# Optimization experiments

Measured on AMD Instinct MI355X. Metric: run time of the kernel, lower is better.

## Reference

```python
import jax, jax.numpy as jnp
import numpy as np

B, S, H = 8, 1024, 1024
NH, HD = 16, 64
LN_EPS = 1e-12


def setup_inputs() -> dict:
    key = jax.random.key(0)
    ks = jax.random.split(key, 8)
    sd = 0.02
    return {
        "hidden_states": jax.random.normal(ks[0], (B, S, H), jnp.float32),
        "attention_mask": jnp.zeros((B, 1, 1, S), jnp.float32),
        "Wq": jax.random.normal(ks[1], (H, H), jnp.float32) * sd,
        "bq": jnp.zeros((H,), jnp.float32),
        "Wk": jax.random.normal(ks[2], (H, H), jnp.float32) * sd,
        "bk": jnp.zeros((H,), jnp.float32),
        "Wv": jax.random.normal(ks[3], (H, H), jnp.float32) * sd,
        "bv": jnp.zeros((H,), jnp.float32),
        "Wo": jax.random.normal(ks[4], (H, H), jnp.float32) * sd,
        "bo": jnp.zeros((H,), jnp.float32),
        "ln_gamma": jnp.ones((H,), jnp.float32),
        "ln_beta": jnp.zeros((H,), jnp.float32),
    }


def _heads(x):
    # [B,S,H] -> [B,NH,S,HD]
    return x.reshape(B, S, NH, HD).transpose(0, 2, 1, 3)


def reference(hidden_states, attention_mask, Wq, bq, Wk, bk, Wv, bv, Wo, bo, ln_gamma, ln_beta):
    # QKV projections (torch Linear: x @ W.T + b)
    q = _heads(hidden_states @ Wq.T + bq)
    k = _heads(hidden_states @ Wk.T + bk)
    v = _heads(hidden_states @ Wv.T + bv)
    # scaled dot-product attention with additive mask
    scores = jnp.einsum("bhqd,bhkd->bhqk", q, k) / np.sqrt(HD).astype(np.float32)
    scores = scores + attention_mask  # broadcast [B,1,1,S]
    probs = jax.nn.softmax(scores, axis=-1)
    ctx = jnp.einsum("bhqk,bhkd->bhqd", probs, v)
    ctx = ctx.transpose(0, 2, 1, 3).reshape(B, S, H)
    # output projection + residual + LayerNorm
    out = ctx @ Wo.T + bo
    x = out + hidden_states
    mu = jnp.mean(x, axis=-1, keepdims=True)
    var = jnp.var(x, axis=-1, keepdims=True)
    return (x - mu) * jax.lax.rsqrt(var + LN_EPS) * ln_gamma + ln_beta
```

## Files before the change

kernel.cpp:

```cpp
#include <hip/hip_runtime.h>
#include <stdint.h>

typedef __attribute__((ext_vector_type(8))) __bf16 bf16x8;
typedef __attribute__((ext_vector_type(8))) unsigned short ushortx8;
typedef __attribute__((ext_vector_type(4))) unsigned short ushortx4;
typedef __attribute__((ext_vector_type(4))) short short4v;
typedef __attribute__((ext_vector_type(4))) float floatx4;

#define LOG2E 1.4426950408889634f
#define QSCALE 0.18033688011112043f

#define ASYNC16(g, l) __builtin_amdgcn_global_load_lds( \
    (__attribute__((address_space(1))) void*)(g),       \
    (__attribute__((address_space(3))) void*)(l), 16, 0, 0)

__device__ __forceinline__ unsigned short f2bf(float f) {
    unsigned int u = __float_as_uint(f);
    u += 0x7fffu + ((u >> 16) & 1u);
    return (unsigned short)(u >> 16);
}

__device__ __forceinline__ floatx4 mfma32(bf16x8 a, bf16x8 b, floatx4 c) {
    return __builtin_amdgcn_mfma_f32_16x16x32_bf16(a, b, c, 0, 0, 0);
}
__device__ __forceinline__ floatx4 mfma16(short4v a, short4v b, floatx4 c) {
    return __builtin_amdgcn_mfma_f32_16x16x16bf16_1k(a, b, c, 0, 0, 0);
}

__global__ __launch_bounds__(256) void cvt_all(
    const float* __restrict__ hidden,
    const float* __restrict__ Wq, const float* __restrict__ Wk,
    const float* __restrict__ Wv, const float* __restrict__ Wo,
    unsigned short* __restrict__ hid_bf,
    unsigned short* __restrict__ oqkv, unsigned short* __restrict__ oo)
{
    const float* src;
    unsigned short* dst;
    int i;
    if (blockIdx.x < 4096) {
        src = hidden; dst = hid_bf;
        i = blockIdx.x * 256 + threadIdx.x;
    } else {
        int blk = (blockIdx.x - 4096) >> 9;
        src = (blk == 0) ? Wq : (blk == 1) ? Wk : (blk == 2) ? Wv : Wo;
        dst = (blk == 3) ? oo : oqkv + (size_t)blk * 1048576;
        i = ((blockIdx.x - 4096) & 511) * 256 + threadIdx.x;
    }
    const float4* p = (const float4*)src + (size_t)i * 2;
    float4 a = p[0], b = p[1];
    ushortx8 o;
    o[0] = f2bf(a.x); o[1] = f2bf(a.y); o[2] = f2bf(a.z); o[3] = f2bf(a.w);
    o[4] = f2bf(b.x); o[5] = f2bf(b.y); o[6] = f2bf(b.z); o[7] = f2bf(b.w);
    *((ushortx8*)dst + i) = o;
}

template<bool SWAP>
__device__ __forceinline__ void kloop_bk64(
    const unsigned short* __restrict__ Ag,
    const unsigned short* __restrict__ Wg,
    unsigned short* As, unsigned short* Bs,
    int wm, int wn, int l16, int quad, int t,
    floatx4 acc[4][4])
{
#pragma unroll 1
    for (int k0 = 0; k0 < 1024; k0 += 64) {
        __syncthreads();
#pragma unroll
        for (int i = 0; i < 4; i++) {
            ASYNC16(Ag + (size_t)i * 32 * 1024 + k0, As + i * 2048 + t * 8);
            ASYNC16(Wg + (size_t)i * 32 * 1024 + k0, Bs + i * 2048 + t * 8);
        }
        __syncthreads();
#pragma unroll
        for (int s = 0; s < 2; s++) {
            int pb = ((s * 4 + quad) ^ (l16 & 7)) * 8;
            bf16x8 af[4], bfr[4];
#pragma unroll
            for (int mt = 0; mt < 4; mt++)
                af[mt] = *(const bf16x8*)(As + (wm + mt * 16 + l16) * 64 + pb);
#pragma unroll
            for (int nt = 0; nt < 4; nt++)
                bfr[nt] = *(const bf16x8*)(Bs + (wn + nt * 16 + l16) * 64 + pb);
            if (SWAP) {
#pragma unroll
                for (int ft = 0; ft < 4; ft++)
#pragma unroll
                    for (int st = 0; st < 4; st++)
                        acc[ft][st] = mfma32(bfr[ft], af[st], acc[ft][st]);
            } else {
#pragma unroll
                for (int mt = 0; mt < 4; mt++)
#pragma unroll
                    for (int nt = 0; nt < 4; nt++)
                        acc[mt][nt] = mfma32(af[mt], bfr[nt], acc[mt][nt]);
            }
        }
    }
}

__global__ __launch_bounds__(256) void gemm_qkv(
    const unsigned short* __restrict__ A,
    const unsigned short* __restrict__ W,
    const float* __restrict__ bq, const float* __restrict__ bk, const float* __restrict__ bv,
    unsigned short* __restrict__ Qo, unsigned short* __restrict__ Ko,
    unsigned short* __restrict__ Vo)
{
    __shared__ unsigned short As[128 * 64];
    __shared__ unsigned short Bs[128 * 64];
    const int t = threadIdx.x;
    const int wave = t >> 6, lane = t & 63;
    const int quad = lane >> 4, l16 = lane & 15;
    const int wm = (wave >> 1) * 64, wn = (wave & 1) * 64;
    const int srow = t >> 3;
    const int scol = ((t & 7) ^ (srow & 7)) * 8;

    const unsigned short* Ag = A + ((size_t)blockIdx.x * 128 + srow) * 1024 + scol;
    const unsigned short* Wg = W + ((size_t)blockIdx.y * 128 + srow) * 1024 + scol;

    floatx4 acc[4][4] = {};
    kloop_bk64<true>(Ag, Wg, As, Bs, wm, wn, l16, quad, t, acc);

    int y = blockIdx.y;
    if (y < 16) {
        const float* bp = (y < 8) ? bq : bk;
        unsigned short* op = (y < 8) ? Qo : Ko;
        float sc = (y < 8) ? QSCALE : 1.0f;
#pragma unroll
        for (int ft = 0; ft < 4; ft++) {
            int featg = (y * 128 + wn + ft * 16 + quad * 4) & 1023;
            float4 b4 = *(const float4*)(bp + featg);
            int h = featg >> 6, d = featg & 63;
#pragma unroll
            for (int st = 0; st < 4; st++) {
                int sg = blockIdx.x * 128 + wm + st * 16 + l16;
                int b = sg >> 10, s = sg & 1023;
                ushortx4 o4;
                o4[0] = f2bf((acc[ft][st][0] + b4.x) * sc);
                o4[1] = f2bf((acc[ft][st][1] + b4.y) * sc);
                o4[2] = f2bf((acc[ft][st][2] + b4.z) * sc);
                o4[3] = f2bf((acc[ft][st][3] + b4.w) * sc);
                *(ushortx4*)(op + (((size_t)(b * 16 + h) * 1024 + s) * 64 + d)) = o4;
            }
        }
    } else {
#pragma unroll
        for (int ft = 0; ft < 4; ft++) {
            int featg = (y * 128 + wn + ft * 16 + quad * 4) & 1023;
            float4 b4 = *(const float4*)(bv + featg);
#pragma unroll
            for (int r = 0; r < 4; r++) {
                int feat = featg + r;
                int h = feat >> 6, d = feat & 63;
                float bias = (r == 0) ? b4.x : (r == 1) ? b4.y : (r == 2) ? b4.z : b4.w;
#pragma unroll
                for (int st = 0; st < 4; st++) {
                    int sg = blockIdx.x * 128 + wm + st * 16 + l16;
                    int b = sg >> 10, s = sg & 1023;
                    int sp = (s & ~63) + (st >> 1) * 32 + (l16 >> 2) * 8 + (st & 1) * 4 + (l16 & 3);
                    Vo[((size_t)(b * 16 + h) * 64 + d) * 1024 + sp] = f2bf(acc[ft][st][r] + bias);
                }
            }
        }
    }
}

__global__ __launch_bounds__(256) void attn(
    const unsigned short* __restrict__ Q,
    const unsigned short* __restrict__ Kg,
    const unsigned short* __restrict__ Vt,
    const float* __restrict__ mask,
    unsigned short* __restrict__ ctx)
{
    __shared__ unsigned short Qs[64 * 64];
    __shared__ unsigned short Ks[64 * 64];
    __shared__ unsigned short Vs[64 * 64];
    __shared__ float Msall[1024];

    const int t = threadIdx.x;
    const int wave = t >> 6, lane = t & 63, quad = lane >> 4, l16 = lane & 15;
    const int s7 = l16 & 7;
    const int head = blockIdx.x;
    const int b = head >> 4, h = head & 15;
    const int q0 = blockIdx.y * 64;
    const unsigned short* Qh = Q + (size_t)head * 65536;
    const unsigned short* Kh = Kg + (size_t)head * 65536;
    const unsigned short* Vh = Vt + (size_t)head * 65536;

    const int srow = t >> 3;
    const int scol = ((t & 7) ^ (srow & 7)) * 8;

    {
        float4 m4 = *(const float4*)(mask + b * 1024 + t * 4);
        m4.x *= LOG2E; m4.y *= LOG2E; m4.z *= LOG2E; m4.w *= LOG2E;
        *(float4*)(Msall + t * 4) = m4;
    }

#pragma unroll
    for (int i = 0; i < 2; i++)
        ASYNC16(Qh + (size_t)(q0 + i * 32 + srow) * 64 + scol, Qs + i * 2048 + t * 8);
    __syncthreads();

    int qrow = wave * 16 + l16;
    bf16x8 qf0 = *(const bf16x8*)(Qs + qrow * 64 + ((quad ^ s7) * 8));
    bf16x8 qf1 = *(const bf16x8*)(Qs + qrow * 64 + (((4 + quad) ^ s7) * 8));

    float rs_acc = 0.f;
    floatx4 o_acc[4] = {};

    for (int k0 = 0; k0 < 1024; k0 += 64) {
        __syncthreads();
#pragma unroll
        for (int i = 0; i < 2; i++) {
            ASYNC16(Kh + (size_t)(k0 + i * 32 + srow) * 64 + scol, Ks + i * 2048 + t * 8);
            ASYNC16(Vh + (size_t)(i * 32 + srow) * 1024 + k0 + scol, Vs + i * 2048 + t * 8);
        }
        __syncthreads();

        short4v pf[4];
#pragma unroll
        for (int nt = 0; nt < 4; nt++) {
            int krow = nt * 16 + l16;
            bf16x8 kf0 = *(const bf16x8*)(Ks + krow * 64 + ((quad ^ s7) * 8));
            bf16x8 kf1 = *(const bf16x8*)(Ks + krow * 64 + (((4 + quad) ^ s7) * 8));
            floatx4 z = {0.f, 0.f, 0.f, 0.f};
            z = mfma32(kf0, qf0, z);
            z = mfma32(kf1, qf1, z);
            floatx4 mk = *(const floatx4*)(Msall + k0 + nt * 16 + quad * 4);
#pragma unroll
            for (int r = 0; r < 4; r++) {
                float p = exp2f(z[r] + mk[r]);
                rs_acc += p;
                pf[nt][r] = (short)(__float_as_uint(p) >> 16);
            }
        }

#pragma unroll
        for (int dt = 0; dt < 4; dt++) {
            int vrow = dt * 16 + l16;
            ushortx8 v01 = *(const ushortx8*)(Vs + vrow * 64 + ((quad ^ s7) * 8));
            ushortx8 v23 = *(const ushortx8*)(Vs + vrow * 64 + (((4 + quad) ^ s7) * 8));
            short4v vf0 = {(short)v01[0], (short)v01[1], (short)v01[2], (short)v01[3]};
            short4v vf1 = {(short)v01[4], (short)v01[5], (short)v01[6], (short)v01[7]};
            short4v vf2 = {(short)v23[0], (short)v23[1], (short)v23[2], (short)v23[3]};
            short4v vf3 = {(short)v23[4], (short)v23[5], (short)v23[6], (short)v23[7]};
            o_acc[dt] = mfma16(vf0, pf[0], o_acc[dt]);
            o_acc[dt] = mfma16(vf1, pf[1], o_acc[dt]);
            o_acc[dt] = mfma16(vf2, pf[2], o_acc[dt]);
            o_acc[dt] = mfma16(vf3, pf[3], o_acc[dt]);
        }
    }

    rs_acc += __shfl_xor(rs_acc, 16);
    rs_acc += __shfl_xor(rs_acc, 32);
    float inv_l = 1.0f / rs_acc;

    int qg = q0 + wave * 16 + l16;
#pragma unroll
    for (int dt = 0; dt < 4; dt++) {
        ushortx4 o4;
#pragma unroll
        for (int r = 0; r < 4; r++) o4[r] = f2bf(o_acc[dt][r] * inv_l);
        *(ushortx4*)(ctx + ((size_t)(b * 1024 + qg)) * 1024 + h * 64 + dt * 16 + quad * 4) = o4;
    }
}

__global__ __launch_bounds__(256) void gemm_proj(
    const unsigned short* __restrict__ A,
    const unsigned short* __restrict__ W,
    const float* __restrict__ bo,
    const float* __restrict__ resid,
    unsigned short* __restrict__ X)
{
    __shared__ unsigned short As[128 * 64];
    __shared__ unsigned short Bs[128 * 64];
    const int t = threadIdx.x;
    const int wave = t >> 6, lane = t & 63;
    const int quad = lane >> 4, l16 = lane & 15;
    const int wm = (wave >> 1) * 64, wn = (wave & 1) * 64;
    const int srow = t >> 3;
    const int scol = ((t & 7) ^ (srow & 7)) * 8;

    const unsigned short* Ag = A + ((size_t)blockIdx.x * 128 + srow) * 1024 + scol;
    const unsigned short* Wg = W + ((size_t)blockIdx.y * 128 + srow) * 1024 + scol;

    floatx4 acc[4][4] = {};
    kloop_bk64<false>(Ag, Wg, As, Bs, wm, wn, l16, quad, t, acc);

#pragma unroll
    for (int nt = 0; nt < 4; nt++) {
        int gn = blockIdx.y * 128 + wn + nt * 16 + l16;
        float bias = bo[gn];
#pragma unroll
        for (int mt = 0; mt < 4; mt++) {
#pragma unroll
            for (int r = 0; r < 4; r++) {
                int gm = blockIdx.x * 128 + wm + mt * 16 + quad * 4 + r;
                size_t off = (size_t)gm * 1024 + gn;
                X[off] = f2bf(acc[mt][nt][r] + bias + resid[off]);
            }
        }
    }
}

__global__ __launch_bounds__(256) void ln_k(const unsigned short* __restrict__ X,
                                            const float* __restrict__ g,
                                            const float* __restrict__ be,
                                            float* __restrict__ out)
{
    int row = blockIdx.x;
    int t = threadIdx.x;
    const unsigned short* xr = X + (size_t)row * 1024;
    ushortx4 xb = *(const ushortx4*)(xr + t * 4);
    float4 v;
    v.x = __uint_as_float((unsigned)xb[0] << 16);
    v.y = __uint_as_float((unsigned)xb[1] << 16);
    v.z = __uint_as_float((unsigned)xb[2] << 16);
    v.w = __uint_as_float((unsigned)xb[3] << 16);
    float s = v.x + v.y + v.z + v.w;
    float ss = v.x * v.x + v.y * v.y + v.z * v.z + v.w * v.w;
    for (int off = 1; off < 64; off <<= 1) {
        s += __shfl_xor(s, off);
        ss += __shfl_xor(ss, off);
    }
    __shared__ float red[8];
    int wave = t >> 6, lane = t & 63;
    if (lane == 0) { red[wave] = s; red[4 + wave] = ss; }
    __syncthreads();
    s = red[0] + red[1] + red[2] + red[3];
    ss = red[4] + red[5] + red[6] + red[7];
    float mu = s * (1.f / 1024.f);
    float var = ss * (1.f / 1024.f) - mu * mu;
    float inv = rsqrtf(var + 1e-12f);
    float4 gv = *(const float4*)(g + t * 4);
    float4 bv = *(const float4*)(be + t * 4);
    float4 o;
    o.x = (v.x - mu) * inv * gv.x + bv.x;
    o.y = (v.y - mu) * inv * gv.y + bv.y;
    o.z = (v.z - mu) * inv * gv.z + bv.z;
    o.w = (v.w - mu) * inv * gv.w + bv.w;
    *(float4*)(out + (size_t)row * 1024 + t * 4) = o;
}

extern "C" void kernel_launch(void* const* d_in, const int* in_sizes, int n_in,
                              void* d_out, int out_size, void* d_ws, size_t ws_size,
                              hipStream_t stream)
{
    const float* hidden = (const float*)d_in[0];
    const float* mask   = (const float*)d_in[1];
    const float* Wq = (const float*)d_in[2];
    const float* bq = (const float*)d_in[3];
    const float* Wk = (const float*)d_in[4];
    const float* bk = (const float*)d_in[5];
    const float* Wv = (const float*)d_in[6];
    const float* bv = (const float*)d_in[7];
    const float* Wo = (const float*)d_in[8];
    const float* bo = (const float*)d_in[9];
    const float* gamma = (const float*)d_in[10];
    const float* beta  = (const float*)d_in[11];
    float* out = (float*)d_out;

    char* ws = (char*)d_ws;
    unsigned short* hid_bf  = (unsigned short*)(ws + 0);
    unsigned short* wqkv_bf = (unsigned short*)(ws + 16777216);
    unsigned short* wo_bf   = (unsigned short*)(ws + 23068672);
    unsigned short* vt_bf   = (unsigned short*)(ws + 25165824);
    unsigned short* ctx_bf  = (unsigned short*)(ws + 41943040);
    unsigned short* q_bf    = (unsigned short*)(ws + 58720256);
    unsigned short* k_bf    = (unsigned short*)(ws + 75497472);
    unsigned short* x_bf    = (unsigned short*)(ws + 58720256);

    cvt_all<<<6144, 256, 0, stream>>>(hidden, Wq, Wk, Wv, Wo, hid_bf, wqkv_bf, wo_bf);

    gemm_qkv<<<dim3(64, 24), 256, 0, stream>>>(hid_bf, wqkv_bf, bq, bk, bv, q_bf, k_bf, vt_bf);
    attn<<<dim3(128, 16), 256, 0, stream>>>(q_bf, k_bf, vt_bf, mask, ctx_bf);
    gemm_proj<<<dim3(64, 8), 256, 0, stream>>>(ctx_bf, wo_bf, bo, hidden, x_bf);
    ln_k<<<8192, 256, 0, stream>>>(x_bf, gamma, beta, out);
}
```

Before: 283.7 us.

## Process 128 queries per attention block and read bf16 residual in projection

Each attention block now handles 128 query rows, with two 16-row query groups per wave, so every K/V tile loaded into LDS is reused across twice as many queries and the grid is halved. Q fragments are loaded straight from global memory into registers instead of being staged through shared memory. The output projection reads the residual from the bf16 copy of hidden_states instead of fp32, halving that read traffic. The cost is more registers per thread, fewer blocks for occupancy, and a bf16-rounded residual that adds a little precision loss.

```diff
diff --git a/kernel.cpp b/kernel.cpp
--- a/kernel.cpp
+++ b/kernel.cpp
@@ -18,6 +18,9 @@
     unsigned int u = __float_as_uint(f);
     u += 0x7fffu + ((u >> 16) & 1u);
     return (unsigned short)(u >> 16);
+}
+__device__ __forceinline__ float bf2f(unsigned short u) {
+    return __uint_as_float((unsigned)u << 16);
 }
 
 __device__ __forceinline__ floatx4 mfma32(bf16x8 a, bf16x8 b, floatx4 c) {
@@ -171,7 +174,6 @@
     const float* __restrict__ mask,
     unsigned short* __restrict__ ctx)
 {
-    __shared__ unsigned short Qs[64 * 64];
     __shared__ unsigned short Ks[64 * 64];
     __shared__ unsigned short Vs[64 * 64];
     __shared__ float Msall[1024];
@@ -181,7 +183,7 @@
     const int s7 = l16 & 7;
     const int head = blockIdx.x;
     const int b = head >> 4, h = head & 15;
-    const int q0 = blockIdx.y * 64;
+    const int q0 = blockIdx.y * 128;
     const unsigned short* Qh = Q + (size_t)head * 65536;
     const unsigned short* Kh = Kg + (size_t)head * 65536;
     const unsigned short* Vh = Vt + (size_t)head * 65536;
@@ -195,17 +197,16 @@
         *(float4*)(Msall + t * 4) = m4;
     }
 
-#pragma unroll
-    for (int i = 0; i < 2; i++)
-        ASYNC16(Qh + (size_t)(q0 + i * 32 + srow) * 64 + scol, Qs + i * 2048 + t * 8);
-    __syncthreads();
-
-    int qrow = wave * 16 + l16;
-    bf16x8 qf0 = *(const bf16x8*)(Qs + qrow * 64 + ((quad ^ s7) * 8));
-    bf16x8 qf1 = *(const bf16x8*)(Qs + qrow * 64 + (((4 + quad) ^ s7) * 8));
-
-    float rs_acc = 0.f;
-    floatx4 o_acc[4] = {};
+    bf16x8 qf[2][2];
+#pragma unroll
+    for (int qg = 0; qg < 2; qg++) {
+        const unsigned short* qp = Qh + (size_t)(q0 + wave * 32 + qg * 16 + l16) * 64 + quad * 8;
+        qf[qg][0] = *(const bf16x8*)(qp);
+        qf[qg][1] = *(const bf16x8*)(qp + 32);
+    }
+
+    float rs0 = 0.f, rs1 = 0.f;
+    floatx4 o_acc[2][4] = {};
 
     for (int k0 = 0; k0 < 1024; k0 += 64) {
         __syncthreads();
@@ -216,21 +217,27 @@
         }
         __syncthreads();
 
-        short4v pf[4];
+        short4v pf0[4], pf1[4];
 #pragma unroll
         for (int nt = 0; nt < 4; nt++) {
             int krow = nt * 16 + l16;
             bf16x8 kf0 = *(const bf16x8*)(Ks + krow * 64 + ((quad ^ s7) * 8));
             bf16x8 kf1 = *(const bf16x8*)(Ks + krow * 64 + (((4 + quad) ^ s7) * 8));
-            floatx4 z = {0.f, 0.f, 0.f, 0.f};
-            z = mfma32(kf0, qf0, z);
-            z = mfma32(kf1, qf1, z);
             floatx4 mk = *(const floatx4*)(Msall + k0 + nt * 16 + quad * 4);
+            floatx4 z0 = {0.f, 0.f, 0.f, 0.f};
+            z0 = mfma32(kf0, qf[0][0], z0);
+            z0 = mfma32(kf1, qf[0][1], z0);
+            floatx4 z1 = {0.f, 0.f, 0.f, 0.f};
+            z1 = mfma32(kf0, qf[1][0], z1);
+            z1 = mfma32(kf1, qf[1][1], z1);
 #pragma unroll
             for (int r = 0; r < 4; r++) {
-                float p = exp2f(z[r] + mk[r]);
-                rs_acc += p;
-                pf[nt][r] = (short)(__float_as_uint(p) >> 16);
+                float p0 = exp2f(z0[r] + mk[r]);
+                float p1 = exp2f(z1[r] + mk[r]);
+                rs0 += p0;
+                rs1 += p1;
+                pf0[nt][r] = (short)(__float_as_uint(p0) >> 16);
+                pf1[nt][r] = (short)(__float_as_uint(p1) >> 16);
             }
         }
 
@@ -243,24 +250,31 @@
             short4v vf1 = {(short)v01[4], (short)v01[5], (short)v01[6], (short)v01[7]};
             short4v vf2 = {(short)v23[0], (short)v23[1], (short)v23[2], (short)v23[3]};
             short4v vf3 = {(short)v23[4], (short)v23[5], (short)v23[6], (short)v23[7]};
-            o_acc[dt] = mfma16(vf0, pf[0], o_acc[dt]);
-            o_acc[dt] = mfma16(vf1, pf[1], o_acc[dt]);
-            o_acc[dt] = mfma16(vf2, pf[2], o_acc[dt]);
-            o_acc[dt] = mfma16(vf3, pf[3], o_acc[dt]);
-        }
-    }
-
-    rs_acc += __shfl_xor(rs_acc, 16);
-    rs_acc += __shfl_xor(rs_acc, 32);
-    float inv_l = 1.0f / rs_acc;
-
-    int qg = q0 + wave * 16 + l16;
-#pragma unroll
-    for (int dt = 0; dt < 4; dt++) {
-        ushortx4 o4;
-#pragma unroll
-        for (int r = 0; r < 4; r++) o4[r] = f2bf(o_acc[dt][r] * inv_l);
-        *(ushortx4*)(ctx + ((size_t)(b * 1024 + qg)) * 1024 + h * 64 + dt * 16 + quad * 4) = o4;
+            o_acc[0][dt] = mfma16(vf0, pf0[0], o_acc[0][dt]);
+            o_acc[0][dt] = mfma16(vf1, pf0[1], o_acc[0][dt]);
+            o_acc[0][dt] = mfma16(vf2, pf0[2], o_acc[0][dt]);
+            o_acc[0][dt] = mfma16(vf3, pf0[3], o_acc[0][dt]);
+            o_acc[1][dt] = mfma16(vf0, pf1[0], o_acc[1][dt]);
+            o_acc[1][dt] = mfma16(vf1, pf1[1], o_acc[1][dt]);
+            o_acc[1][dt] = mfma16(vf2, pf1[2], o_acc[1][dt]);
+            o_acc[1][dt] = mfma16(vf3, pf1[3], o_acc[1][dt]);
+        }
+    }
+
+#pragma unroll
+    for (int qg = 0; qg < 2; qg++) {
+        float v = (qg == 0) ? rs0 : rs1;
+        v += __shfl_xor(v, 16);
+        v += __shfl_xor(v, 32);
+        float inv_l = 1.0f / v;
+        int qrow = q0 + wave * 32 + qg * 16 + l16;
+#pragma unroll
+        for (int dt = 0; dt < 4; dt++) {
+            ushortx4 o4;
+#pragma unroll
+            for (int r = 0; r < 4; r++) o4[r] = f2bf(o_acc[qg][dt][r] * inv_l);
+            *(ushortx4*)(ctx + ((size_t)(b * 1024 + qrow)) * 1024 + h * 64 + dt * 16 + quad * 4) = o4;
+        }
     }
 }
 
@@ -268,7 +282,7 @@
     const unsigned short* __restrict__ A,
     const unsigned short* __restrict__ W,
     const float* __restrict__ bo,
-    const float* __restrict__ resid,
+    const unsigned short* __restrict__ resid,
     unsigned short* __restrict__ X)
 {
     __shared__ unsigned short As[128 * 64];
@@ -296,7 +310,7 @@
             for (int r = 0; r < 4; r++) {
                 int gm = blockIdx.x * 128 + wm + mt * 16 + quad * 4 + r;
                 size_t off = (size_t)gm * 1024 + gn;
-                X[off] = f2bf(acc[mt][nt][r] + bias + resid[off]);
+                X[off] = f2bf(acc[mt][nt][r] + bias + bf2f(resid[off]));
             }
         }
     }
@@ -312,10 +326,10 @@
     const unsigned short* xr = X + (size_t)row * 1024;
     ushortx4 xb = *(const ushortx4*)(xr + t * 4);
     float4 v;
-    v.x = __uint_as_float((unsigned)xb[0] << 16);
-    v.y = __uint_as_float((unsigned)xb[1] << 16);
-    v.z = __uint_as_float((unsigned)xb[2] << 16);
-    v.w = __uint_as_float((unsigned)xb[3] << 16);
+    v.x = bf2f(xb[0]);
+    v.y = bf2f(xb[1]);
+    v.z = bf2f(xb[2]);
+    v.w = bf2f(xb[3]);
     float s = v.x + v.y + v.z + v.w;
     float ss = v.x * v.x + v.y * v.y + v.z * v.z + v.w * v.w;
     for (int off = 1; off < 64; off <<= 1) {
@@ -372,7 +386,7 @@
     cvt_all<<<6144, 256, 0, stream>>>(hidden, Wq, Wk, Wv, Wo, hid_bf, wqkv_bf, wo_bf);
 
     gemm_qkv<<<dim3(64, 24), 256, 0, stream>>>(hid_bf, wqkv_bf, bq, bk, bv, q_bf, k_bf, vt_bf);
-    attn<<<dim3(128, 16), 256, 0, stream>>>(q_bf, k_bf, vt_bf, mask, ctx_bf);
-    gemm_proj<<<dim3(64, 8), 256, 0, stream>>>(ctx_bf, wo_bf, bo, hidden, x_bf);
+    attn<<<dim3(128, 8), 256, 0, stream>>>(q_bf, k_bf, vt_bf, mask, ctx_bf);
+    gemm_proj<<<dim3(64, 8), 256, 0, stream>>>(ctx_bf, wo_bf, bo, hid_bf, x_bf);
     ln_k<<<8192, 256, 0, stream>>>(x_bf, gamma, beta, out);
 }
```

Result: faster. 270.9 us (-4.5%).
